# Performance work log

Hardware: AMD Instinct MI355X
Metric: run time of the kernel (lower is better)

Reference implementation:

```python
import jax, jax.numpy as jnp
import numpy as np

N_ENTITY = 100000
N_RELATION = 32
DIM = 64
N_LAYER = 2
B = 4096
T = 32


def _knowledge_attention(h_set, path, t_emb, W1, W2):
    # h_set, path, t_emb: [B, T, D]
    x = jnp.concatenate([h_set, path], axis=-1)          # [B, T, 2D]
    a = jax.nn.sigmoid(jax.nn.sigmoid(x @ W1) @ W2)      # [B, T]
    w = jax.nn.softmax(a, axis=-1)                       # softmax over triples
    return jnp.einsum('bt,btd->bd', w, t_emb)            # [B, D]


def _branch(h_idx, r_idx, t_idx, ent, rel, W1, W2):
    # h_idx/r_idx/t_idx: [L, B, T] ints. Faithful to the original loop,
    # which re-adds layer-i head emb and re-multiplies layer-i relation emb i times.
    outs = []
    for i in range(N_LAYER):
        h_set = ent[h_idx[0]]                            # [B, T, D]
        path = rel[r_idx[0]]                             # [B, T, D]
        for _k in range(1, i + 1):
            h_set = h_set + ent[h_idx[i]]
            path = path * rel[r_idx[i]]
        outs.append(_knowledge_attention(h_set, path, ent[t_idx[i]], W1, W2))
    return outs


def setup_inputs() -> dict:
    key = jax.random.key(0)
    ks = jax.random.split(key, 20)
    d = {}
    d['items'] = jax.random.randint(ks[0], (B,), 0, N_ENTITY)
    names = ['uis', 'ipt', 'upt', 'iot']
    i = 1
    for nm in names:
        d[nm + '_h'] = jax.random.randint(ks[i], (N_LAYER, B, T), 0, N_ENTITY); i += 1
        d[nm + '_r'] = jax.random.randint(ks[i], (N_LAYER, B, T), 0, N_RELATION); i += 1
        d[nm + '_t'] = jax.random.randint(ks[i], (N_LAYER, B, T), 0, N_ENTITY); i += 1
    # xavier-ish scales
    d['ent_emb'] = jax.random.normal(ks[13], (N_ENTITY, DIM), jnp.float32) * 0.05
    d['rel_emb'] = jax.random.normal(ks[14], (N_RELATION, DIM), jnp.float32) * 0.05
    d['W1'] = jax.random.normal(ks[15], (2 * DIM, DIM), jnp.float32) * (1.0 / np.sqrt(2 * DIM))
    d['W2'] = jax.random.normal(ks[16], (DIM,), jnp.float32) * (1.0 / np.sqrt(DIM))
    return d


def reference(items, uis_h, uis_r, uis_t, ipt_h, ipt_r, ipt_t,
              upt_h, upt_r, upt_t, iot_h, iot_r, iot_t,
              ent_emb, rel_emb, W1, W2):
    # user embeddings (init triple set)
    user_embs = [ent_emb[uis_h[0]].mean(axis=1)]
    user_embs += _branch(uis_h, uis_r, uis_t, ent_emb, rel_emb, W1, W2)
    # item embeddings (potential triple set)
    item_embs = [ent_emb[items]]
    item_embs += _branch(ipt_h, ipt_r, ipt_t, ent_emb, rel_emb, W1, W2)
    # user potential embeddings
    upo_embs = [ent_emb[upt_h[0]].mean(axis=1)]
    upo_embs += _branch(upt_h, upt_r, upt_t, ent_emb, rel_emb, W1, W2)
    # item origin embeddings
    ior_embs = [ent_emb[iot_h[0]].mean(axis=1)]
    ior_embs += _branch(iot_h, iot_r, iot_t, ent_emb, rel_emb, W1, W2)
    # agg == 'sum': extra item term appended before predict
    item_embs.append(ent_emb[ipt_h[0]].mean(axis=1))
    e_u = sum(user_embs[1:], user_embs[0])
    e_i = sum(item_embs[1:], item_embs[0])
    e_p_u = sum(upo_embs[1:], upo_embs[0])
    e_p_i = sum(ior_embs[1:], ior_embs[0])
    e_u = jnp.concatenate([e_u, e_p_u], axis=-1)
    e_i = jnp.concatenate([e_p_i, e_i], axis=-1)
    scores = jax.nn.sigmoid((e_i * e_u).sum(axis=1))     # [B]
    kge_loss = jnp.float32(0.0)                          # agg='sum' path: no SSL loss
    return scores, kge_loss
```

## Files before the change

### kernel.cpp

```cpp
#include <hip/hip_runtime.h>


#define NE   100000
#define NR   32
#define DIMD 64
#define BB   4096
#define TT   32
#define BT   (BB * TT)

__device__ __forceinline__ float sigf(float x) { return 1.0f / (1.0f + __expf(-x)); }
__device__ __forceinline__ float4 ld4(const float* p) {
    return *reinterpret_cast<const float4*>(p);
}

__device__ __forceinline__ float b2f(unsigned short u) {
    return __builtin_bit_cast(float, ((unsigned)u) << 16);
}
__device__ __forceinline__ unsigned short f2b(float x) {
    unsigned b = __builtin_bit_cast(unsigned, x);
    b += 0x7FFF + ((b >> 16) & 1);
    return (unsigned short)(b >> 16);
}
__device__ __forceinline__ float4 ldb4(const unsigned short* p) {
    ushort4 v = *reinterpret_cast<const ushort4*>(p);
    return make_float4(b2f(v.x), b2f(v.y), b2f(v.z), b2f(v.w));
}

template <int CTRL>
__device__ __forceinline__ float dpp_add(float x) {
    int r = __builtin_amdgcn_update_dpp(0, __builtin_bit_cast(int, x), CTRL,
                                        0xf, 0xf, true);
    return x + __builtin_bit_cast(float, r);
}
__device__ __forceinline__ float reduce16(float x) {
    x = dpp_add<0x121>(x);
    x = dpp_add<0x122>(x);
    x = dpp_add<0x124>(x);
    x = dpp_add<0x128>(x);
    return x;
}

__global__ __launch_bounds__(256) void k_proj_ent(const float* __restrict__ ent,
                                                  const float* __restrict__ W1,
                                                  unsigned short* __restrict__ tab) {
    __shared__ float sW[64][68];
    __shared__ float sR[64][68];
    const int tid = threadIdx.x;
    const int row0 = blockIdx.x * 64;

#pragma unroll
    for (int i = 0; i < 4; ++i) {
        const int idx = tid + 256 * i;
        const int r = idx >> 4;
        const int c = idx & 15;
        const float4 wv = ld4(W1 + r * DIMD + 4 * c);
        sW[r][4 * c + 0] = wv.x; sW[r][4 * c + 1] = wv.y;
        sW[r][4 * c + 2] = wv.z; sW[r][4 * c + 3] = wv.w;
        const int er = (row0 + r < NE) ? (row0 + r) : (NE - 1);
        const float4 rv = ld4(ent + er * DIMD + 4 * c);
        sR[r][4 * c + 0] = rv.x; sR[r][4 * c + 1] = rv.y;
        sR[r][4 * c + 2] = rv.z; sR[r][4 * c + 3] = rv.w;
    }
    __syncthreads();

    const int q = tid & 15;
    const int trow = tid >> 4;
    float4 acc0 = make_float4(0.f, 0.f, 0.f, 0.f);
    float4 acc1 = acc0, acc2 = acc0, acc3 = acc0;

#pragma unroll
    for (int kk = 0; kk < 16; ++kk) {
        const float4 r0 = ld4(&sR[4 * trow + 0][4 * kk]);
        const float4 r1 = ld4(&sR[4 * trow + 1][4 * kk]);
        const float4 r2 = ld4(&sR[4 * trow + 2][4 * kk]);
        const float4 r3 = ld4(&sR[4 * trow + 3][4 * kk]);
#pragma unroll
        for (int i = 0; i < 4; ++i) {
            const float4 wv = ld4(&sW[4 * kk + i][4 * q]);
            const float s0 = (i == 0) ? r0.x : (i == 1) ? r0.y : (i == 2) ? r0.z : r0.w;
            const float s1 = (i == 0) ? r1.x : (i == 1) ? r1.y : (i == 2) ? r1.z : r1.w;
            const float s2 = (i == 0) ? r2.x : (i == 1) ? r2.y : (i == 2) ? r2.z : r2.w;
            const float s3 = (i == 0) ? r3.x : (i == 1) ? r3.y : (i == 2) ? r3.z : r3.w;
            acc0.x = fmaf(s0, wv.x, acc0.x); acc0.y = fmaf(s0, wv.y, acc0.y);
            acc0.z = fmaf(s0, wv.z, acc0.z); acc0.w = fmaf(s0, wv.w, acc0.w);
            acc1.x = fmaf(s1, wv.x, acc1.x); acc1.y = fmaf(s1, wv.y, acc1.y);
            acc1.z = fmaf(s1, wv.z, acc1.z); acc1.w = fmaf(s1, wv.w, acc1.w);
            acc2.x = fmaf(s2, wv.x, acc2.x); acc2.y = fmaf(s2, wv.y, acc2.y);
            acc2.z = fmaf(s2, wv.z, acc2.z); acc2.w = fmaf(s2, wv.w, acc2.w);
            acc3.x = fmaf(s3, wv.x, acc3.x); acc3.y = fmaf(s3, wv.y, acc3.y);
            acc3.z = fmaf(s3, wv.z, acc3.z); acc3.w = fmaf(s3, wv.w, acc3.w);
        }
    }

    const int orow = row0 + 4 * trow;
#pragma unroll
    for (int i = 0; i < 4; ++i) {
        if (orow + i < NE) {
            const float4 a = (i == 0) ? acc0 : (i == 1) ? acc1 : (i == 2) ? acc2 : acc3;
            unsigned short* rowp = tab + ((size_t)(orow + i) << 7);
            ushort4 ev, pv;
            ev.x = f2b(sR[4 * trow + i][4 * q + 0]);
            ev.y = f2b(sR[4 * trow + i][4 * q + 1]);
            ev.z = f2b(sR[4 * trow + i][4 * q + 2]);
            ev.w = f2b(sR[4 * trow + i][4 * q + 3]);
            pv.x = f2b(a.x); pv.y = f2b(a.y); pv.z = f2b(a.z); pv.w = f2b(a.w);
            *reinterpret_cast<ushort4*>(rowp + 4 * q) = ev;
            *reinterpret_cast<ushort4*>(rowp + 64 + 4 * q) = pv;
        }
    }
}

__global__ __launch_bounds__(256) void k_proj_rel(const float* __restrict__ rel,
                                                  const float* __restrict__ W1,
                                                  float* __restrict__ Prel1,
                                                  float* __restrict__ Prel2) {
    int gid = blockIdx.x * 256 + threadIdx.x;
    int row = gid >> 6;
    int d = gid & 63;
    if (row < 1024) {
        const float* a = rel + (row >> 5) * DIMD;
        const float* c = rel + (row & 31) * DIMD;
        float acc = 0.0f;
#pragma unroll
        for (int k = 0; k < DIMD; ++k)
            acc = fmaf(a[k] * c[k], W1[(DIMD + k) * DIMD + d], acc);
        Prel2[row * DIMD + d] = acc;
    } else if (row < 1056) {
        const float* a = rel + (row - 1024) * DIMD;
        float acc = 0.0f;
#pragma unroll
        for (int k = 0; k < DIMD; ++k)
            acc = fmaf(a[k], W1[(DIMD + k) * DIMD + d], acc);
        Prel1[(row - 1024) * DIMD + d] = acc;
    }
}

__global__ __launch_bounds__(256) void k_main(
    const int* __restrict__ items,
    const int* __restrict__ uh, const int* __restrict__ ur, const int* __restrict__ ut,
    const int* __restrict__ ih, const int* __restrict__ ir, const int* __restrict__ itp,
    const int* __restrict__ ph, const int* __restrict__ pr, const int* __restrict__ pt,
    const int* __restrict__ oh, const int* __restrict__ orr, const int* __restrict__ ot,
    const unsigned short* __restrict__ tab,
    const float* __restrict__ W2,
    const float* __restrict__ Prel1, const float* __restrict__ Prel2,
    float* __restrict__ out) {
    const int b = blockIdx.x;
    const int tid = threadIdx.x;
    const int w = tid >> 6;
    const int lane = tid & 63;
    const int g = lane >> 4;
    const int q = lane & 15;

    const int* hp;
    const int* rp;
    const int* tp;
    switch (w) {
        case 0: hp = uh; rp = ur; tp = ut; break;
        case 1: hp = ih; rp = ir; tp = itp; break;
        case 2: hp = ph; rp = pr; tp = pt; break;
        default: hp = oh; rp = orr; tp = ot; break;
    }

    __shared__ int sidx[4][3][2][TT];
    {
        const int l = lane >> 5;
        const int t0 = lane & 31;
        const int off = l * BT + b * TT + t0;
        sidx[w][0][l][t0] = hp[off];
        sidx[w][1][l][t0] = rp[off];
        sidx[w][2][l][t0] = tp[off];
    }
    const int item_idx = (w == 1) ? items[b] : 0;

    const float4 w2v = ld4(W2 + 4 * q);

    float d0[8], d1[8];
    float4 accH = make_float4(0.f, 0.f, 0.f, 0.f);
#pragma unroll
    for (int p = 0; p < 8; ++p) {
        const int t = 4 * p + g;
        const int ih0 = sidx[w][0][0][t];
        const int ih1 = sidx[w][0][1][t];
        const int ir0 = sidx[w][1][0][t];
        const int ir1 = sidx[w][1][1][t];
        const unsigned short* row0p = tab + ((size_t)ih0 << 7);
        const float4 H  = ldb4(row0p + 4 * q);
        const float4 A0 = ldb4(row0p + 64 + 4 * q);
        const float4 A1 = ldb4(tab + ((size_t)ih1 << 7) + 64 + 4 * q);
        const float4 R0 = ld4(Prel1 + (ir0 << 6) + 4 * q);
        const float4 R2 = ld4(Prel2 + ((ir0 * 32 + ir1) << 6) + 4 * q);

        accH.x += H.x; accH.y += H.y; accH.z += H.z; accH.w += H.w;

        float v = sigf(A0.x + R0.x) * w2v.x;
        v = fmaf(sigf(A0.y + R0.y), w2v.y, v);
        v = fmaf(sigf(A0.z + R0.z), w2v.z, v);
        v = fmaf(sigf(A0.w + R0.w), w2v.w, v);
        d0[p] = v;

        float u = sigf(A0.x + A1.x + R2.x) * w2v.x;
        u = fmaf(sigf(A0.y + A1.y + R2.y), w2v.y, u);
        u = fmaf(sigf(A0.z + A1.z + R2.z), w2v.z, u);
        u = fmaf(sigf(A0.w + A1.w + R2.w), w2v.w, u);
        d1[p] = u;
    }

    float e0[8], e1[8];
    float s0 = 0.0f, s1 = 0.0f;
#pragma unroll
    for (int p = 0; p < 8; ++p) {
        e0[p] = __expf(sigf(reduce16(d0[p])));
        e1[p] = __expf(sigf(reduce16(d1[p])));
        s0 += e0[p];
        s1 += e1[p];
    }
    s0 += __shfl_xor(s0, 16, 64);
    s0 += __shfl_xor(s0, 32, 64);
    s1 += __shfl_xor(s1, 16, 64);
    s1 += __shfl_xor(s1, 32, 64);

    float4 acc0 = make_float4(0.f, 0.f, 0.f, 0.f);
    float4 acc1 = acc0;
#pragma unroll
    for (int p = 0; p < 8; ++p) {
        const int t = 4 * p + g;
        const int it0 = sidx[w][2][0][t];
        const int it1 = sidx[w][2][1][t];
        const float4 T0 = ldb4(tab + ((size_t)it0 << 7) + 4 * q);
        const float4 T1 = ldb4(tab + ((size_t)it1 << 7) + 4 * q);
        acc0.x = fmaf(e0[p], T0.x, acc0.x); acc0.y = fmaf(e0[p], T0.y, acc0.y);
        acc0.z = fmaf(e0[p], T0.z, acc0.z); acc0.w = fmaf(e0[p], T0.w, acc0.w);
        acc1.x = fmaf(e1[p], T1.x, acc1.x); acc1.y = fmaf(e1[p], T1.y, acc1.y);
        acc1.z = fmaf(e1[p], T1.z, acc1.z); acc1.w = fmaf(e1[p], T1.w, acc1.w);
    }

    const float inv0 = 1.0f / s0;
    const float inv1 = 1.0f / s1;
    float4 v;
    v.x = fmaf(acc0.x, inv0, fmaf(acc1.x, inv1, 0.03125f * accH.x));
    v.y = fmaf(acc0.y, inv0, fmaf(acc1.y, inv1, 0.03125f * accH.y));
    v.z = fmaf(acc0.z, inv0, fmaf(acc1.z, inv1, 0.03125f * accH.z));
    v.w = fmaf(acc0.w, inv0, fmaf(acc1.w, inv1, 0.03125f * accH.w));

    v.x += __shfl_xor(v.x, 16, 64); v.x += __shfl_xor(v.x, 32, 64);
    v.y += __shfl_xor(v.y, 16, 64); v.y += __shfl_xor(v.y, 32, 64);
    v.z += __shfl_xor(v.z, 16, 64); v.z += __shfl_xor(v.z, 32, 64);
    v.w += __shfl_xor(v.w, 16, 64); v.w += __shfl_xor(v.w, 32, 64);

    if (w == 1) {
        const float4 iv = ldb4(tab + ((size_t)item_idx << 7) + 4 * q);
        v.x += iv.x; v.y += iv.y; v.z += iv.z; v.w += iv.w;
    }

    __shared__ float vec[4][DIMD];
    if (g == 0) {
        vec[w][4 * q + 0] = v.x;
        vec[w][4 * q + 1] = v.y;
        vec[w][4 * q + 2] = v.z;
        vec[w][4 * q + 3] = v.w;
    }
    __syncthreads();

    if (tid < 64) {
        float z = fmaf(vec[0][tid], vec[3][tid], vec[2][tid] * vec[1][tid]);
#pragma unroll
        for (int m = 1; m < 64; m <<= 1) z += __shfl_xor(z, m, 64);
        if (tid == 0) out[b] = sigf(z);
    }
    if (b == 0 && tid == 0) out[BB] = 0.0f;
}

extern "C" void kernel_launch(void* const* d_in, const int* in_sizes, int n_in,
                              void* d_out, int out_size, void* d_ws, size_t ws_size,
                              hipStream_t stream) {
    const int* items = (const int*)d_in[0];
    const int* uh = (const int*)d_in[1];
    const int* ur = (const int*)d_in[2];
    const int* ut = (const int*)d_in[3];
    const int* ih = (const int*)d_in[4];
    const int* ir = (const int*)d_in[5];
    const int* itp = (const int*)d_in[6];
    const int* ph = (const int*)d_in[7];
    const int* pr = (const int*)d_in[8];
    const int* pt = (const int*)d_in[9];
    const int* oh = (const int*)d_in[10];
    const int* orr = (const int*)d_in[11];
    const int* ot = (const int*)d_in[12];
    const float* ent = (const float*)d_in[13];
    const float* rel = (const float*)d_in[14];
    const float* W1 = (const float*)d_in[15];
    const float* W2 = (const float*)d_in[16];
    float* out = (float*)d_out;

    float* Prel1 = (float*)d_ws;
    float* Prel2 = Prel1 + NR * DIMD;
    unsigned short* tab =
        (unsigned short*)(Prel2 + 1024 * DIMD);

    hipLaunchKernelGGL(k_proj_ent, dim3((NE + 63) / 64), dim3(256), 0, stream,
                       ent, W1, tab);
    hipLaunchKernelGGL(k_proj_rel, dim3((1056 * 64 + 255) / 256), dim3(256), 0,
                       stream, rel, W1, Prel1, Prel2);
    hipLaunchKernelGGL(k_main, dim3(BB), dim3(256), 0, stream, items, uh, ur, ut,
                       ih, ir, itp, ph, pr, pt, oh, orr, ot, tab, W2, Prel1,
                       Prel2, out);
}
```

Baseline: 197.2 us.

## Batch gathers ahead of compute, store relation tables in bf16, drop W1 LDS staging

In the main kernel, all gather loads (head, projected-head, relation and tail rows) are now issued up front into register arrays, so many independent memory requests are in flight before any arithmetic starts. Tail and item rows are loaded before the softmax math to hide their latency. The projected relation tables are packed into one bf16 buffer to halve their load bytes. In the entity projection kernel W1 is read straight from global memory instead of being staged in LDS. This raises register pressure and may lower occupancy, and bf16 relation projections lose some precision.

```diff
diff --git a/kernel.cpp b/kernel.cpp
--- a/kernel.cpp
+++ b/kernel.cpp
@@ -21,9 +21,11 @@
     b += 0x7FFF + ((b >> 16) & 1);
     return (unsigned short)(b >> 16);
 }
-__device__ __forceinline__ float4 ldb4(const unsigned short* p) {
-    ushort4 v = *reinterpret_cast<const ushort4*>(p);
+__device__ __forceinline__ float4 u2f4(ushort4 v) {
     return make_float4(b2f(v.x), b2f(v.y), b2f(v.z), b2f(v.w));
+}
+__device__ __forceinline__ ushort4 ldu4(const unsigned short* p) {
+    return *reinterpret_cast<const ushort4*>(p);
 }
 
 template <int CTRL>
@@ -43,7 +45,6 @@
 __global__ __launch_bounds__(256) void k_proj_ent(const float* __restrict__ ent,
                                                   const float* __restrict__ W1,
                                                   unsigned short* __restrict__ tab) {
-    __shared__ float sW[64][68];
     __shared__ float sR[64][68];
     const int tid = threadIdx.x;
     const int row0 = blockIdx.x * 64;
@@ -53,9 +54,6 @@
         const int idx = tid + 256 * i;
         const int r = idx >> 4;
         const int c = idx & 15;
-        const float4 wv = ld4(W1 + r * DIMD + 4 * c);
-        sW[r][4 * c + 0] = wv.x; sW[r][4 * c + 1] = wv.y;
-        sW[r][4 * c + 2] = wv.z; sW[r][4 * c + 3] = wv.w;
         const int er = (row0 + r < NE) ? (row0 + r) : (NE - 1);
         const float4 rv = ld4(ent + er * DIMD + 4 * c);
         sR[r][4 * c + 0] = rv.x; sR[r][4 * c + 1] = rv.y;
@@ -76,7 +74,7 @@
         const float4 r3 = ld4(&sR[4 * trow + 3][4 * kk]);
 #pragma unroll
         for (int i = 0; i < 4; ++i) {
-            const float4 wv = ld4(&sW[4 * kk + i][4 * q]);
+            const float4 wv = ld4(W1 + (4 * kk + i) * DIMD + 4 * q);
             const float s0 = (i == 0) ? r0.x : (i == 1) ? r0.y : (i == 2) ? r0.z : r0.w;
             const float s1 = (i == 0) ? r1.x : (i == 1) ? r1.y : (i == 2) ? r1.z : r1.w;
             const float s2 = (i == 0) ? r2.x : (i == 1) ? r2.y : (i == 2) ? r2.z : r2.w;
@@ -112,26 +110,26 @@
 
 __global__ __launch_bounds__(256) void k_proj_rel(const float* __restrict__ rel,
                                                   const float* __restrict__ W1,
-                                                  float* __restrict__ Prel1,
-                                                  float* __restrict__ Prel2) {
+                                                  unsigned short* __restrict__ relB) {
     int gid = blockIdx.x * 256 + threadIdx.x;
     int row = gid >> 6;
     int d = gid & 63;
-    if (row < 1024) {
-        const float* a = rel + (row >> 5) * DIMD;
-        const float* c = rel + (row & 31) * DIMD;
+    if (row < 32) {
+        const float* a = rel + row * DIMD;
+        float acc = 0.0f;
+#pragma unroll
+        for (int k = 0; k < DIMD; ++k)
+            acc = fmaf(a[k], W1[(DIMD + k) * DIMD + d], acc);
+        relB[row * DIMD + d] = f2b(acc);
+    } else if (row < 32 + 1024) {
+        const int rr = row - 32;
+        const float* a = rel + (rr >> 5) * DIMD;
+        const float* c = rel + (rr & 31) * DIMD;
         float acc = 0.0f;
 #pragma unroll
         for (int k = 0; k < DIMD; ++k)
             acc = fmaf(a[k] * c[k], W1[(DIMD + k) * DIMD + d], acc);
-        Prel2[row * DIMD + d] = acc;
-    } else if (row < 1056) {
-        const float* a = rel + (row - 1024) * DIMD;
-        float acc = 0.0f;
-#pragma unroll
-        for (int k = 0; k < DIMD; ++k)
-            acc = fmaf(a[k], W1[(DIMD + k) * DIMD + d], acc);
-        Prel1[(row - 1024) * DIMD + d] = acc;
+        relB[row * DIMD + d] = f2b(acc);
     }
 }
 
@@ -142,8 +140,8 @@
     const int* __restrict__ ph, const int* __restrict__ pr, const int* __restrict__ pt,
     const int* __restrict__ oh, const int* __restrict__ orr, const int* __restrict__ ot,
     const unsigned short* __restrict__ tab,
+    const unsigned short* __restrict__ relB,
     const float* __restrict__ W2,
-    const float* __restrict__ Prel1, const float* __restrict__ Prel2,
     float* __restrict__ out) {
     const int b = blockIdx.x;
     const int tid = threadIdx.x;
@@ -173,23 +171,40 @@
     }
     const int item_idx = (w == 1) ? items[b] : 0;
 
+    int jh0[8], jh1[8], jr0[8], jr1[8], jt0[8], jt1[8];
+#pragma unroll
+    for (int p = 0; p < 8; ++p) {
+        const int t = 4 * p + g;
+        jh0[p] = sidx[w][0][0][t];
+        jh1[p] = sidx[w][0][1][t];
+        jr0[p] = sidx[w][1][0][t];
+        jr1[p] = sidx[w][1][1][t];
+        jt0[p] = sidx[w][2][0][t];
+        jt1[p] = sidx[w][2][1][t];
+    }
+
+    ushort4 rH[8], rA0[8], rA1[8], rR0[8], rR2[8];
+#pragma unroll
+    for (int p = 0; p < 8; ++p) {
+        const unsigned short* r0p = tab + ((size_t)jh0[p] << 7) + 4 * q;
+        rH[p] = ldu4(r0p);
+        rA0[p] = ldu4(r0p + 64);
+        rA1[p] = ldu4(tab + ((size_t)jh1[p] << 7) + 64 + 4 * q);
+        rR0[p] = ldu4(relB + ((size_t)jr0[p] << 6) + 4 * q);
+        rR2[p] = ldu4(relB + ((size_t)(32 + jr0[p] * 32 + jr1[p]) << 6) + 4 * q);
+    }
+
     const float4 w2v = ld4(W2 + 4 * q);
 
     float d0[8], d1[8];
     float4 accH = make_float4(0.f, 0.f, 0.f, 0.f);
 #pragma unroll
     for (int p = 0; p < 8; ++p) {
-        const int t = 4 * p + g;
-        const int ih0 = sidx[w][0][0][t];
-        const int ih1 = sidx[w][0][1][t];
-        const int ir0 = sidx[w][1][0][t];
-        const int ir1 = sidx[w][1][1][t];
-        const unsigned short* row0p = tab + ((size_t)ih0 << 7);
-        const float4 H  = ldb4(row0p + 4 * q);
-        const float4 A0 = ldb4(row0p + 64 + 4 * q);
-        const float4 A1 = ldb4(tab + ((size_t)ih1 << 7) + 64 + 4 * q);
-        const float4 R0 = ld4(Prel1 + (ir0 << 6) + 4 * q);
-        const float4 R2 = ld4(Prel2 + ((ir0 * 32 + ir1) << 6) + 4 * q);
+        const float4 H = u2f4(rH[p]);
+        const float4 A0 = u2f4(rA0[p]);
+        const float4 A1 = u2f4(rA1[p]);
+        const float4 R0 = u2f4(rR0[p]);
+        const float4 R2 = u2f4(rR2[p]);
 
         accH.x += H.x; accH.y += H.y; accH.z += H.z; accH.w += H.w;
 
@@ -206,6 +221,14 @@
         d1[p] = u;
     }
 
+    ushort4 rT0[8], rT1[8];
+#pragma unroll
+    for (int p = 0; p < 8; ++p) {
+        rT0[p] = ldu4(tab + ((size_t)jt0[p] << 7) + 4 * q);
+        rT1[p] = ldu4(tab + ((size_t)jt1[p] << 7) + 4 * q);
+    }
+    const ushort4 rIt = ldu4(tab + ((size_t)item_idx << 7) + 4 * q);
+
     float e0[8], e1[8];
     float s0 = 0.0f, s1 = 0.0f;
 #pragma unroll
@@ -224,11 +247,8 @@
     float4 acc1 = acc0;
 #pragma unroll
     for (int p = 0; p < 8; ++p) {
-        const int t = 4 * p + g;
-        const int it0 = sidx[w][2][0][t];
-        const int it1 = sidx[w][2][1][t];
-        const float4 T0 = ldb4(tab + ((size_t)it0 << 7) + 4 * q);
-        const float4 T1 = ldb4(tab + ((size_t)it1 << 7) + 4 * q);
+        const float4 T0 = u2f4(rT0[p]);
+        const float4 T1 = u2f4(rT1[p]);
         acc0.x = fmaf(e0[p], T0.x, acc0.x); acc0.y = fmaf(e0[p], T0.y, acc0.y);
         acc0.z = fmaf(e0[p], T0.z, acc0.z); acc0.w = fmaf(e0[p], T0.w, acc0.w);
         acc1.x = fmaf(e1[p], T1.x, acc1.x); acc1.y = fmaf(e1[p], T1.y, acc1.y);
@@ -249,7 +269,7 @@
     v.w += __shfl_xor(v.w, 16, 64); v.w += __shfl_xor(v.w, 32, 64);
 
     if (w == 1) {
-        const float4 iv = ldb4(tab + ((size_t)item_idx << 7) + 4 * q);
+        const float4 iv = u2f4(rIt);
         v.x += iv.x; v.y += iv.y; v.z += iv.z; v.w += iv.w;
     }
 
@@ -293,16 +313,13 @@
     const float* W2 = (const float*)d_in[16];
     float* out = (float*)d_out;
 
-    float* Prel1 = (float*)d_ws;
-    float* Prel2 = Prel1 + NR * DIMD;
-    unsigned short* tab =
-        (unsigned short*)(Prel2 + 1024 * DIMD);
+    unsigned short* relB = (unsigned short*)d_ws;
+    unsigned short* tab = relB + 1056 * DIMD;
 
     hipLaunchKernelGGL(k_proj_ent, dim3((NE + 63) / 64), dim3(256), 0, stream,
                        ent, W1, tab);
     hipLaunchKernelGGL(k_proj_rel, dim3((1056 * 64 + 255) / 256), dim3(256), 0,
-                       stream, rel, W1, Prel1, Prel2);
+                       stream, rel, W1, relB);
     hipLaunchKernelGGL(k_main, dim3(BB), dim3(256), 0, stream, items, uh, ur, ut,
-                       ih, ir, itp, ph, pr, pt, oh, orr, ot, tab, W2, Prel1,
-                       Prel2, out);
-}
+                       ih, ir, itp, ph, pr, pt, oh, orr, ot, tab, relB, W2, out);
+}
```

Result: slower. 202.4 us (+2.6%).
